# Kernel tuning notes

Hardware: AMD Instinct MI355X
Metric: run time of the kernel (lower is better)

## Reference

```python
import jax, jax.numpy as jnp
from jax import lax
import numpy as np

V, E, H, L, B, ML, T = 32000, 512, 512, 2, 64, 64, 32


def setup_inputs() -> dict:
    key = jax.random.key(0)
    ks = jax.random.split(key, 16)
    s = 0.05
    return {
        "current_input": jax.random.randint(ks[0], (B,), 0, V),
        "h0": jax.random.normal(ks[1], (L, B, H), jnp.float32),
        "c0": jax.random.normal(ks[2], (L, B, H), jnp.float32),
        "encoder_output": jax.random.normal(ks[3], (ML, B, H), jnp.float32),
        "gtruth": jax.random.randint(ks[4], (T, B), 0, V),
        "length": T,
        "emb": s * jax.random.normal(ks[5], (V, E), jnp.float32),
        "attn_W": s * jax.random.normal(ks[6], (ML, E + H), jnp.float32),
        "attn_out_W": s * jax.random.normal(ks[7], (E, E + H), jnp.float32),
        "lstm_Wi": s * jax.random.normal(ks[8], (L, 4 * H, E), jnp.float32),
        "lstm_Wh": s * jax.random.normal(ks[9], (L, 4 * H, H), jnp.float32),
        "lstm_bi": s * jax.random.normal(ks[10], (L, 4 * H), jnp.float32),
        "lstm_bh": s * jax.random.normal(ks[11], (L, 4 * H), jnp.float32),
        "gen_W": s * jax.random.normal(ks[12], (V, H), jnp.float32),
        "gen_b": s * jax.random.normal(ks[13], (V,), jnp.float32),
    }


def _lstm_cell(x, h, c, Wi, Wh, bi, bh):
    # PyTorch gate order: i, f, g, o
    g = x @ Wi.T + h @ Wh.T + bi + bh  # [B, 4H]
    i, f, gg, o = jnp.split(g, 4, axis=-1)
    c_new = jax.nn.sigmoid(f) * c + jax.nn.sigmoid(i) * jnp.tanh(gg)
    h_new = jax.nn.sigmoid(o) * jnp.tanh(c_new)
    return h_new, c_new


def reference(current_input, h0, c0, encoder_output, gtruth, length,
              emb, attn_W, attn_out_W, lstm_Wi, lstm_Wh, lstm_bi, lstm_bh,
              gen_W, gen_b):
    n_layers = h0.shape[0]

    def step_fn(carry, tok):
        h, c = carry  # each [L, B, H]
        emb_t = emb[tok]                                   # [B, E]
        attn_in = jnp.concatenate([emb_t, h[-1]], axis=1)  # [B, E+H]
        a = jax.nn.softmax(attn_in @ attn_W.T, axis=1)     # [B, ML]
        ctx = jnp.einsum('bl,lbh->bh', a, encoder_output)  # [B, H]
        rnn_in = jax.nn.relu(
            jnp.concatenate([emb_t, ctx], axis=1) @ attn_out_W.T)  # [B, E]
        x = rnn_in
        hs, cs = [], []
        for l in range(n_layers):
            hn, cn = _lstm_cell(x, h[l], c[l], lstm_Wi[l], lstm_Wh[l],
                                lstm_bi[l], lstm_bh[l])
            hs.append(hn)
            cs.append(cn)
            x = hn
        scores = x @ gen_W.T + gen_b  # [B, V]
        return (jnp.stack(hs), jnp.stack(cs)), scores

    # teacher forcing: step t consumes current_input at t=0, gtruth[t-1] after
    tokens = jnp.concatenate([current_input[None], gtruth[:-1]], axis=0)  # [T, B]
    (h_fin, c_fin), outputs = lax.scan(step_fn, (h0, c0), tokens)
    return outputs, h_fin, c_fin
```

## Files before the change

kernel.cpp:

```cpp
#include <hip/hip_runtime.h>
#include <hip/hip_bf16.h>

typedef __bf16 bf16_t;
typedef bf16_t bf16x8 __attribute__((ext_vector_type(8)));
typedef float f32x4 __attribute__((ext_vector_type(4)));

#define MFMA(a, b, c) __builtin_amdgcn_mfma_f32_16x16x32_bf16((a), (b), (c), 0, 0, 0)

__device__ __forceinline__ float sigm(float x) { return 1.f / (1.f + __expf(-x)); }
__device__ __forceinline__ float tanh_f(float x) { return 1.f - 2.f / (__expf(2.f * x) + 1.f); }

__device__ __forceinline__ bf16x8 cvt8(const float* p) {
    f32x4 a = *(const f32x4*)p, b = *(const f32x4*)(p + 4);
    bf16x8 v;
#pragma unroll
    for (int i = 0; i < 4; ++i) { v[i] = (bf16_t)a[i]; v[4 + i] = (bf16_t)b[i]; }
    return v;
}

__global__ void k_cvt(const float* __restrict__ src, bf16_t* __restrict__ dst, int n) {
    int i = (blockIdx.x * 256 + threadIdx.x) * 8;
    if (i < n) *(bf16x8*)(dst + i) = cvt8(src + i);
}

__global__ void k_init(const float* __restrict__ h0, const float* __restrict__ c0,
                       const float* __restrict__ bi, const float* __restrict__ bh,
                       float* __restrict__ c_f32, bf16_t* __restrict__ h_bf,
                       float* __restrict__ bsum) {
    int idx = blockIdx.x * 256 + threadIdx.x;
    if (idx < 65536) { c_f32[idx] = c0[idx]; h_bf[idx] = (bf16_t)h0[idx]; }
    if (idx < 4096) bsum[idx] = bi[idx] + bh[idx];
}

__global__ __launch_bounds__(256) void k_pre(const float* __restrict__ emb,
                                             const int* __restrict__ cur, const int* __restrict__ gt,
                                             const bf16_t* __restrict__ Bm, int ldb, int koff,
                                             float* __restrict__ out, int ldo) {
    int tid = threadIdx.x, lane = tid & 63, w = tid >> 6;
    int m = lane & 15, q = lane >> 4;
    int mrow = blockIdx.x * 64 + w * 16 + m;
    int tok = (mrow < 64) ? cur[mrow] : gt[mrow - 64];
    const float* arow = emb + (size_t)tok * 512;
    int n0 = blockIdx.y * 64;
    const bf16_t* brow0 = Bm + (size_t)(n0 + m) * ldb + koff;
    f32x4 acc[4] = {};
    for (int ks = 0; ks < 16; ++ks) {
        int kc = ks * 32 + q * 8;
        bf16x8 a = cvt8(arow + kc);
#pragma unroll
        for (int nt = 0; nt < 4; ++nt) {
            bf16x8 b = *(const bf16x8*)(brow0 + (size_t)nt * 16 * ldb + kc);
            acc[nt] = MFMA(a, b, acc[nt]);
        }
    }
    int rbase = blockIdx.x * 64 + w * 16 + q * 4;
#pragma unroll
    for (int nt = 0; nt < 4; ++nt)
#pragma unroll
        for (int i = 0; i < 4; ++i)
            out[(size_t)(rbase + i) * ldo + n0 + nt * 16 + m] = acc[nt][i];
}

__global__ __launch_bounds__(256) void k_attn_rnn(int t, const bf16_t* __restrict__ h2,
                                                  const bf16_t* __restrict__ attn_W,
                                                  const bf16_t* __restrict__ attn_out_W,
                                                  const float* __restrict__ enc,
                                                  const float* __restrict__ pre_s,
                                                  const float* __restrict__ pre_r,
                                                  bf16_t* __restrict__ rnn_bf) {
    __shared__ float s_p[8][64];
    __shared__ bf16_t s_ctx[16][520];
    int tid = threadIdx.x, lane = tid & 63, w = tid >> 6;
    int m = lane & 15, q = lane >> 4;
    int b0 = blockIdx.x * 8;
    for (int i = tid; i < 8 * 520; i += 256) s_ctx[8 + i / 520][i % 520] = (bf16_t)0.f;
    {
        const bf16_t* aptr = h2 + (size_t)(b0 + (m & 7)) * 512;
        const bf16_t* bptr = attn_W + (size_t)(w * 16 + m) * 1024 + 512;
        f32x4 acc = {};
        for (int ks = 0; ks < 16; ++ks) {
            int kc = ks * 32 + q * 8;
            acc = MFMA(*(const bf16x8*)(aptr + kc), *(const bf16x8*)(bptr + kc), acc);
        }
#pragma unroll
        for (int i = 0; i < 4; ++i) {
            int mr = q * 4 + i;
            if (mr < 8)
                s_p[mr][w * 16 + m] = acc[i] + pre_s[((size_t)t * 64 + b0 + mr) * 64 + w * 16 + m];
        }
    }
    __syncthreads();
    if (tid < 8) {
        float mx = -1e30f;
        for (int l = 0; l < 64; ++l) mx = fmaxf(mx, s_p[tid][l]);
        float sum = 0.f;
        for (int l = 0; l < 64; ++l) { float e = __expf(s_p[tid][l] - mx); s_p[tid][l] = e; sum += e; }
        float inv = 1.f / sum;
        for (int l = 0; l < 64; ++l) s_p[tid][l] *= inv;
    }
    __syncthreads();
    {
        int b = tid >> 5, g = tid & 31, h0 = g * 16;
        float acc[16];
#pragma unroll
        for (int i = 0; i < 16; ++i) acc[i] = 0.f;
        const float* ebase = enc + (size_t)(b0 + b) * 512 + h0;
        for (int l = 0; l < 64; ++l) {
            float a = s_p[b][l];
            const float* e = ebase + (size_t)l * 32768;
            f32x4 e0 = *(const f32x4*)(e), e1 = *(const f32x4*)(e + 4);
            f32x4 e2 = *(const f32x4*)(e + 8), e3 = *(const f32x4*)(e + 12);
#pragma unroll
            for (int i = 0; i < 4; ++i) {
                acc[i] += a * e0[i]; acc[4 + i] += a * e1[i];
                acc[8 + i] += a * e2[i]; acc[12 + i] += a * e3[i];
            }
        }
#pragma unroll
        for (int i = 0; i < 16; ++i) s_ctx[b][h0 + i] = (bf16_t)acc[i];
    }
    __syncthreads();
    {
        f32x4 acc[8] = {};
        const bf16_t* actx = &s_ctx[m][0];
        const bf16_t* bbase = attn_out_W + (size_t)(w * 128 + m) * 1024 + 512;
        for (int ks = 0; ks < 16; ++ks) {
            int kc = ks * 32 + q * 8;
            bf16x8 a = *(const bf16x8*)(actx + kc);
#pragma unroll
            for (int nt = 0; nt < 8; ++nt) {
                bf16x8 b = *(const bf16x8*)(bbase + (size_t)nt * 16 * 1024 + kc);
                acc[nt] = MFMA(a, b, acc[nt]);
            }
        }
#pragma unroll
        for (int nt = 0; nt < 8; ++nt)
#pragma unroll
            for (int i = 0; i < 4; ++i) {
                int mr = q * 4 + i;
                if (mr < 8) {
                    int b = b0 + mr, j = w * 128 + nt * 16 + m;
                    float v = acc[nt][i] + pre_r[((size_t)t * 64 + b) * 512 + j];
                    rnn_bf[(size_t)b * 512 + j] = (bf16_t)fmaxf(v, 0.f);
                }
            }
    }
}

__global__ __launch_bounds__(256) void k_lstm(const bf16_t* __restrict__ x,
                                              const bf16_t* __restrict__ hprev,
                                              const bf16_t* __restrict__ Wi,
                                              const bf16_t* __restrict__ Wh,
                                              const float* __restrict__ bsum,
                                              float* __restrict__ c,
                                              bf16_t* __restrict__ hout,
                                              bf16_t* __restrict__ xs_out) {
    int tid = threadIdx.x, lane = tid & 63, w = tid >> 6;
    int m = lane & 15, q = lane >> 4;
    int j0 = blockIdx.x * 16;
    const bf16_t* ax = x + (size_t)(w * 16 + m) * 512;
    const bf16_t* ah = hprev + (size_t)(w * 16 + m) * 512;
    f32x4 acc[4] = {};
    for (int ks = 0; ks < 16; ++ks) {
        int kc = ks * 32 + q * 8;
        bf16x8 a = *(const bf16x8*)(ax + kc);
#pragma unroll
        for (int g = 0; g < 4; ++g) {
            const bf16_t* bp = Wi + (size_t)(g * 512 + j0 + m) * 512 + kc;
            acc[g] = MFMA(a, *(const bf16x8*)bp, acc[g]);
        }
    }
    for (int ks = 0; ks < 16; ++ks) {
        int kc = ks * 32 + q * 8;
        bf16x8 a = *(const bf16x8*)(ah + kc);
#pragma unroll
        for (int g = 0; g < 4; ++g) {
            const bf16_t* bp = Wh + (size_t)(g * 512 + j0 + m) * 512 + kc;
            acc[g] = MFMA(a, *(const bf16x8*)bp, acc[g]);
        }
    }
    int j = j0 + m;
    float bs0 = bsum[j], bs1 = bsum[512 + j], bs2 = bsum[1024 + j], bs3 = bsum[1536 + j];
#pragma unroll
    for (int i = 0; i < 4; ++i) {
        int b = w * 16 + q * 4 + i;
        float ig = acc[0][i] + bs0;
        float fg = acc[1][i] + bs1;
        float gg = acc[2][i] + bs2;
        float og = acc[3][i] + bs3;
        size_t off = (size_t)b * 512 + j;
        float co = c[off];
        float cn = sigm(fg) * co + sigm(ig) * tanh_f(gg);
        float hn = sigm(og) * tanh_f(cn);
        c[off] = cn;
        hout[off] = (bf16_t)hn;
        if (xs_out) xs_out[off] = (bf16_t)hn;
    }
}

__global__ __launch_bounds__(256) void k_gen(const bf16_t* __restrict__ xs,
                                             const bf16_t* __restrict__ gen_W,
                                             const float* __restrict__ gen_b,
                                             float* __restrict__ out) {
    __shared__ bf16_t sA[64 * 256];
    int tid = threadIdx.x, lane = tid & 63, w = tid >> 6;
    int m = lane & 15, q4 = lane >> 4;
    int m0 = blockIdx.x * 64, n0 = blockIdx.y * 256;
    f32x4 acc[4][4] = {};
    for (int ko = 0; ko < 2; ++ko) {
        __syncthreads();
#pragma unroll
        for (int it = 0; it < 8; ++it) {
            int idx = it * 256 + tid;
            int mr = idx >> 5, qc = idx & 31;
            bf16x8 v = *(const bf16x8*)(xs + (size_t)(m0 + mr) * 512 + ko * 256 + qc * 8);
            *(bf16x8*)(&sA[(mr * 32 + (qc ^ (mr & 7))) * 8]) = v;
        }
        __syncthreads();
        const bf16_t* bbase = gen_W + (size_t)(n0 + w * 64 + m) * 512 + ko * 256;
        for (int ks = 0; ks < 8; ++ks) {
            bf16x8 af[4];
#pragma unroll
            for (int mt = 0; mt < 4; ++mt) {
                int r = mt * 16 + m, chunk = ks * 4 + q4;
                af[mt] = *(const bf16x8*)(&sA[(r * 32 + (chunk ^ (r & 7))) * 8]);
            }
            int kc = ks * 32 + q4 * 8;
#pragma unroll
            for (int nt = 0; nt < 4; ++nt) {
                bf16x8 bfrag = *(const bf16x8*)(bbase + (size_t)nt * 16 * 512 + kc);
#pragma unroll
                for (int mt = 0; mt < 4; ++mt) acc[mt][nt] = MFMA(af[mt], bfrag, acc[mt][nt]);
            }
        }
    }
#pragma unroll
    for (int nt = 0; nt < 4; ++nt) {
        int col = n0 + w * 64 + nt * 16 + m;
        float bias = gen_b[col];
#pragma unroll
        for (int mt = 0; mt < 4; ++mt)
#pragma unroll
            for (int i = 0; i < 4; ++i) {
                int r = m0 + mt * 16 + q4 * 4 + i;
                out[(size_t)r * 32000 + col] = acc[mt][nt][i] + bias;
            }
    }
}

__global__ void k_tail(const bf16_t* __restrict__ h_bf0, const float* __restrict__ c_f32,
                       float* __restrict__ out) {
    int idx = blockIdx.x * 256 + threadIdx.x;
    if (idx < 65536) {
        out[65536000 + idx] = (float)h_bf0[idx];
        out[65601536 + idx] = c_f32[idx];
    }
}

extern "C" void kernel_launch(void* const* d_in, const int* in_sizes, int n_in,
                              void* d_out, int out_size, void* d_ws, size_t ws_size,
                              hipStream_t stream) {
    const int* cur = (const int*)d_in[0];
    const float* h0 = (const float*)d_in[1];
    const float* c0 = (const float*)d_in[2];
    const float* enc = (const float*)d_in[3];
    const int* gt = (const int*)d_in[4];
    const float* emb = (const float*)d_in[6];
    const float* attn_W = (const float*)d_in[7];
    const float* attn_out_W = (const float*)d_in[8];
    const float* Wi = (const float*)d_in[9];
    const float* Wh = (const float*)d_in[10];
    const float* bi = (const float*)d_in[11];
    const float* bh = (const float*)d_in[12];
    const float* gen_W = (const float*)d_in[13];
    const float* gen_b = (const float*)d_in[14];
    float* out = (float*)d_out;

    char* ws = (char*)d_ws;
    float* c_f32 = (float*)(ws + 0);
    bf16_t* h_bf = (bf16_t*)(ws + 262144);
    float* bsum = (float*)(ws + 524288);
    float* pre_s = (float*)(ws + 540672);
    float* pre_r = (float*)(ws + 1064960);
    bf16_t* rnn_bf = (bf16_t*)(ws + 5259264);
    bf16_t* xs = (bf16_t*)(ws + 5324800);
    bf16_t* attn_W_bf = (bf16_t*)(ws + 7421952);
    bf16_t* attn_out_W_bf = (bf16_t*)(ws + 7553024);
    bf16_t* Wi_bf = (bf16_t*)(ws + 8601600);
    bf16_t* Wh_bf = (bf16_t*)(ws + 12795904);
    bf16_t* gen_W_bf = (bf16_t*)(ws + 16990208);

    k_cvt<<<32, 256, 0, stream>>>(attn_W, attn_W_bf, 65536);
    k_cvt<<<256, 256, 0, stream>>>(attn_out_W, attn_out_W_bf, 524288);
    k_cvt<<<1024, 256, 0, stream>>>(Wi, Wi_bf, 2097152);
    k_cvt<<<1024, 256, 0, stream>>>(Wh, Wh_bf, 2097152);
    k_cvt<<<8000, 256, 0, stream>>>(gen_W, gen_W_bf, 16384000);
    k_init<<<256, 256, 0, stream>>>(h0, c0, bi, bh, c_f32, h_bf, bsum);
    k_pre<<<dim3(32, 1), 256, 0, stream>>>(emb, cur, gt, attn_W_bf, 1024, 0, pre_s, 64);
    k_pre<<<dim3(32, 8), 256, 0, stream>>>(emb, cur, gt, attn_out_W_bf, 1024, 0, pre_r, 512);

    for (int t = 0; t < 32; ++t) {
        int p = t & 1;
        const bf16_t* hp = h_bf + (size_t)p * 65536;
        bf16_t* hn = h_bf + (size_t)(p ^ 1) * 65536;
        k_attn_rnn<<<8, 256, 0, stream>>>(t, hp + 32768, attn_W_bf, attn_out_W_bf, enc, pre_s, pre_r, rnn_bf);
        k_lstm<<<32, 256, 0, stream>>>(rnn_bf, hp, Wi_bf, Wh_bf, bsum, c_f32, hn, nullptr);
        k_lstm<<<32, 256, 0, stream>>>(hn, hp + 32768, Wi_bf + 1048576, Wh_bf + 1048576, bsum + 2048,
                                       c_f32 + 32768, hn + 32768, xs + (size_t)t * 32768);
    }
    k_gen<<<dim3(32, 125), 256, 0, stream>>>(xs, gen_W_bf, gen_b, out);
    k_tail<<<256, 256, 0, stream>>>(h_bf, c_f32, out);
}
```

Baseline: 3.295 ms.

## Fuse recurrent time loop into one persistent kernel with grid barriers

Replaces the 96 per-step kernel launches (attention, two LSTM layers) with a single persistent 32-block kernel. Blocks synchronize through an atomic-counter global barrier between phases. The attention work is repartitioned so each block handles 2 batch rows for softmax/context and a 16-column slice of the attn_out projection, with the context staged through a global buffer. It also uses wave shuffles for the softmax. This removes launch gaps and tail effects, at the cost of four grid-wide barriers per step and a reliance on all 32 blocks being co-resident.

```diff
diff --git a/kernel.cpp b/kernel.cpp
--- a/kernel.cpp
+++ b/kernel.cpp
@@ -3,6 +3,7 @@
 
 typedef __bf16 bf16_t;
 typedef bf16_t bf16x8 __attribute__((ext_vector_type(8)));
+typedef bf16_t bf16x4 __attribute__((ext_vector_type(4)));
 typedef float f32x4 __attribute__((ext_vector_type(4)));
 
 #define MFMA(a, b, c) __builtin_amdgcn_mfma_f32_16x16x32_bf16((a), (b), (c), 0, 0, 0)
@@ -18,6 +19,18 @@
     return v;
 }
 
+__device__ __forceinline__ void gbar(int* cnt, int target) {
+    __syncthreads();
+    if (threadIdx.x == 0) {
+        __threadfence();
+        __hip_atomic_fetch_add(cnt, 1, __ATOMIC_RELEASE, __HIP_MEMORY_SCOPE_AGENT);
+        while (__hip_atomic_load(cnt, __ATOMIC_ACQUIRE, __HIP_MEMORY_SCOPE_AGENT) < target)
+            __builtin_amdgcn_s_sleep(2);
+        __threadfence();
+    }
+    __syncthreads();
+}
+
 __global__ void k_cvt(const float* __restrict__ src, bf16_t* __restrict__ dst, int n) {
     int i = (blockIdx.x * 256 + threadIdx.x) * 8;
     if (i < n) *(bf16x8*)(dst + i) = cvt8(src + i);
@@ -26,10 +39,11 @@
 __global__ void k_init(const float* __restrict__ h0, const float* __restrict__ c0,
                        const float* __restrict__ bi, const float* __restrict__ bh,
                        float* __restrict__ c_f32, bf16_t* __restrict__ h_bf,
-                       float* __restrict__ bsum) {
+                       float* __restrict__ bsum, int* __restrict__ bar) {
     int idx = blockIdx.x * 256 + threadIdx.x;
     if (idx < 65536) { c_f32[idx] = c0[idx]; h_bf[idx] = (bf16_t)h0[idx]; }
     if (idx < 4096) bsum[idx] = bi[idx] + bh[idx];
+    if (idx == 0) *bar = 0;
 }
 
 __global__ __launch_bounds__(256) void k_pre(const float* __restrict__ emb,
@@ -61,103 +75,18 @@
             out[(size_t)(rbase + i) * ldo + n0 + nt * 16 + m] = acc[nt][i];
 }
 
-__global__ __launch_bounds__(256) void k_attn_rnn(int t, const bf16_t* __restrict__ h2,
-                                                  const bf16_t* __restrict__ attn_W,
-                                                  const bf16_t* __restrict__ attn_out_W,
-                                                  const float* __restrict__ enc,
-                                                  const float* __restrict__ pre_s,
-                                                  const float* __restrict__ pre_r,
-                                                  bf16_t* __restrict__ rnn_bf) {
-    __shared__ float s_p[8][64];
-    __shared__ bf16_t s_ctx[16][520];
-    int tid = threadIdx.x, lane = tid & 63, w = tid >> 6;
+__device__ __forceinline__ void lstm_phase(int wg, int tid,
+                                           const bf16_t* __restrict__ x,
+                                           const bf16_t* __restrict__ hprev,
+                                           const bf16_t* __restrict__ Wi,
+                                           const bf16_t* __restrict__ Wh,
+                                           const float* __restrict__ bsum,
+                                           float* __restrict__ c,
+                                           bf16_t* __restrict__ hout,
+                                           bf16_t* __restrict__ xs_out) {
+    int lane = tid & 63, w = tid >> 6;
     int m = lane & 15, q = lane >> 4;
-    int b0 = blockIdx.x * 8;
-    for (int i = tid; i < 8 * 520; i += 256) s_ctx[8 + i / 520][i % 520] = (bf16_t)0.f;
-    {
-        const bf16_t* aptr = h2 + (size_t)(b0 + (m & 7)) * 512;
-        const bf16_t* bptr = attn_W + (size_t)(w * 16 + m) * 1024 + 512;
-        f32x4 acc = {};
-        for (int ks = 0; ks < 16; ++ks) {
-            int kc = ks * 32 + q * 8;
-            acc = MFMA(*(const bf16x8*)(aptr + kc), *(const bf16x8*)(bptr + kc), acc);
-        }
-#pragma unroll
-        for (int i = 0; i < 4; ++i) {
-            int mr = q * 4 + i;
-            if (mr < 8)
-                s_p[mr][w * 16 + m] = acc[i] + pre_s[((size_t)t * 64 + b0 + mr) * 64 + w * 16 + m];
-        }
-    }
-    __syncthreads();
-    if (tid < 8) {
-        float mx = -1e30f;
-        for (int l = 0; l < 64; ++l) mx = fmaxf(mx, s_p[tid][l]);
-        float sum = 0.f;
-        for (int l = 0; l < 64; ++l) { float e = __expf(s_p[tid][l] - mx); s_p[tid][l] = e; sum += e; }
-        float inv = 1.f / sum;
-        for (int l = 0; l < 64; ++l) s_p[tid][l] *= inv;
-    }
-    __syncthreads();
-    {
-        int b = tid >> 5, g = tid & 31, h0 = g * 16;
-        float acc[16];
-#pragma unroll
-        for (int i = 0; i < 16; ++i) acc[i] = 0.f;
-        const float* ebase = enc + (size_t)(b0 + b) * 512 + h0;
-        for (int l = 0; l < 64; ++l) {
-            float a = s_p[b][l];
-            const float* e = ebase + (size_t)l * 32768;
-            f32x4 e0 = *(const f32x4*)(e), e1 = *(const f32x4*)(e + 4);
-            f32x4 e2 = *(const f32x4*)(e + 8), e3 = *(const f32x4*)(e + 12);
-#pragma unroll
-            for (int i = 0; i < 4; ++i) {
-                acc[i] += a * e0[i]; acc[4 + i] += a * e1[i];
-                acc[8 + i] += a * e2[i]; acc[12 + i] += a * e3[i];
-            }
-        }
-#pragma unroll
-        for (int i = 0; i < 16; ++i) s_ctx[b][h0 + i] = (bf16_t)acc[i];
-    }
-    __syncthreads();
-    {
-        f32x4 acc[8] = {};
-        const bf16_t* actx = &s_ctx[m][0];
-        const bf16_t* bbase = attn_out_W + (size_t)(w * 128 + m) * 1024 + 512;
-        for (int ks = 0; ks < 16; ++ks) {
-            int kc = ks * 32 + q * 8;
-            bf16x8 a = *(const bf16x8*)(actx + kc);
-#pragma unroll
-            for (int nt = 0; nt < 8; ++nt) {
-                bf16x8 b = *(const bf16x8*)(bbase + (size_t)nt * 16 * 1024 + kc);
-                acc[nt] = MFMA(a, b, acc[nt]);
-            }
-        }
-#pragma unroll
-        for (int nt = 0; nt < 8; ++nt)
-#pragma unroll
-            for (int i = 0; i < 4; ++i) {
-                int mr = q * 4 + i;
-                if (mr < 8) {
-                    int b = b0 + mr, j = w * 128 + nt * 16 + m;
-                    float v = acc[nt][i] + pre_r[((size_t)t * 64 + b) * 512 + j];
-                    rnn_bf[(size_t)b * 512 + j] = (bf16_t)fmaxf(v, 0.f);
-                }
-            }
-    }
-}
-
-__global__ __launch_bounds__(256) void k_lstm(const bf16_t* __restrict__ x,
-                                              const bf16_t* __restrict__ hprev,
-                                              const bf16_t* __restrict__ Wi,
-                                              const bf16_t* __restrict__ Wh,
-                                              const float* __restrict__ bsum,
-                                              float* __restrict__ c,
-                                              bf16_t* __restrict__ hout,
-                                              bf16_t* __restrict__ xs_out) {
-    int tid = threadIdx.x, lane = tid & 63, w = tid >> 6;
-    int m = lane & 15, q = lane >> 4;
-    int j0 = blockIdx.x * 16;
+    int j0 = wg * 16;
     const bf16_t* ax = x + (size_t)(w * 16 + m) * 512;
     const bf16_t* ah = hprev + (size_t)(w * 16 + m) * 512;
     f32x4 acc[4] = {};
@@ -195,6 +124,109 @@
         c[off] = cn;
         hout[off] = (bf16_t)hn;
         if (xs_out) xs_out[off] = (bf16_t)hn;
+    }
+}
+
+__global__ __launch_bounds__(256) void k_loop(const bf16_t* __restrict__ attn_W_bf,
+                                              const bf16_t* __restrict__ attn_out_W_bf,
+                                              const float* __restrict__ enc,
+                                              const float* __restrict__ pre_s,
+                                              const float* __restrict__ pre_r,
+                                              const bf16_t* __restrict__ Wi_bf,
+                                              const bf16_t* __restrict__ Wh_bf,
+                                              const float* __restrict__ bsum,
+                                              float* __restrict__ c_f32,
+                                              bf16_t* __restrict__ h_bf,
+                                              bf16_t* __restrict__ ctx_bf,
+                                              bf16_t* __restrict__ rnn_bf,
+                                              bf16_t* __restrict__ xs,
+                                              int* __restrict__ bar) {
+    __shared__ float s_p[2][64];
+    int tid = threadIdx.x, lane = tid & 63, w = tid >> 6;
+    int m = lane & 15, q = lane >> 4;
+    int wg = blockIdx.x;
+    int b0 = wg * 2;
+    int bt = 0;
+
+    for (int t = 0; t < 32; ++t) {
+        int p = t & 1;
+        const bf16_t* h1p = h_bf + (size_t)p * 65536;
+        const bf16_t* h2p = h1p + 32768;
+        bf16_t* h1n = h_bf + (size_t)(p ^ 1) * 65536;
+        bf16_t* h2n = h1n + 32768;
+
+        {
+            const bf16_t* aptr = h2p + (size_t)(b0 + (m & 1)) * 512;
+            const bf16_t* bptr = attn_W_bf + (size_t)(w * 16 + m) * 1024 + 512;
+            f32x4 acc = {};
+            for (int ks = 0; ks < 16; ++ks) {
+                int kc = ks * 32 + q * 8;
+                acc = MFMA(*(const bf16x8*)(aptr + kc), *(const bf16x8*)(bptr + kc), acc);
+            }
+            if (q == 0) {
+#pragma unroll
+                for (int i = 0; i < 2; ++i)
+                    s_p[i][w * 16 + m] =
+                        acc[i] + pre_s[((size_t)t * 64 + b0 + i) * 64 + w * 16 + m];
+            }
+        }
+        __syncthreads();
+        if (tid < 128) {
+            int r = tid >> 6, l = tid & 63;
+            float v = s_p[r][l];
+            float mx = v;
+#pragma unroll
+            for (int off = 32; off; off >>= 1) mx = fmaxf(mx, __shfl_xor(mx, off));
+            float e = __expf(v - mx);
+            float s = e;
+#pragma unroll
+            for (int off = 32; off; off >>= 1) s += __shfl_xor(s, off);
+            s_p[r][l] = e / s;
+        }
+        __syncthreads();
+        {
+            int r = tid >> 7, c0 = (tid & 127) * 4;
+            int b = b0 + r;
+            f32x4 acc = {};
+            const float* ebase = enc + (size_t)b * 512 + c0;
+            for (int l = 0; l < 64; ++l) {
+                float a = s_p[r][l];
+                f32x4 e = *(const f32x4*)(ebase + (size_t)l * 32768);
+#pragma unroll
+                for (int i = 0; i < 4; ++i) acc[i] += a * e[i];
+            }
+            bf16x4 cv;
+#pragma unroll
+            for (int i = 0; i < 4; ++i) cv[i] = (bf16_t)acc[i];
+            *(bf16x4*)(ctx_bf + (size_t)b * 512 + c0) = cv;
+        }
+        bt += 32; gbar(bar, bt);
+
+        {
+            int j0 = wg * 16;
+            const bf16_t* actx = ctx_bf + (size_t)(w * 16 + m) * 512;
+            const bf16_t* bptr = attn_out_W_bf + (size_t)(j0 + m) * 1024 + 512;
+            f32x4 acc = {};
+            for (int ks = 0; ks < 16; ++ks) {
+                int kc = ks * 32 + q * 8;
+                acc = MFMA(*(const bf16x8*)(actx + kc), *(const bf16x8*)(bptr + kc), acc);
+            }
+            int jj = j0 + m;
+#pragma unroll
+            for (int i = 0; i < 4; ++i) {
+                int b = w * 16 + q * 4 + i;
+                float v = acc[i] + pre_r[((size_t)t * 64 + b) * 512 + jj];
+                rnn_bf[(size_t)b * 512 + jj] = (bf16_t)fmaxf(v, 0.f);
+            }
+        }
+        bt += 32; gbar(bar, bt);
+
+        lstm_phase(wg, tid, rnn_bf, h1p, Wi_bf, Wh_bf, bsum, c_f32, h1n, nullptr);
+        bt += 32; gbar(bar, bt);
+
+        lstm_phase(wg, tid, h1n, h2p, Wi_bf + 1048576, Wh_bf + 1048576, bsum + 2048,
+                   c_f32 + 32768, h2n, xs + (size_t)t * 32768);
+        bt += 32; gbar(bar, bt);
     }
 }
 
@@ -289,25 +321,21 @@
     bf16_t* Wi_bf = (bf16_t*)(ws + 8601600);
     bf16_t* Wh_bf = (bf16_t*)(ws + 12795904);
     bf16_t* gen_W_bf = (bf16_t*)(ws + 16990208);
+    bf16_t* ctx_bf = (bf16_t*)(ws + 49758208);
+    int* bar = (int*)(ws + 49823744);
 
     k_cvt<<<32, 256, 0, stream>>>(attn_W, attn_W_bf, 65536);
     k_cvt<<<256, 256, 0, stream>>>(attn_out_W, attn_out_W_bf, 524288);
     k_cvt<<<1024, 256, 0, stream>>>(Wi, Wi_bf, 2097152);
     k_cvt<<<1024, 256, 0, stream>>>(Wh, Wh_bf, 2097152);
     k_cvt<<<8000, 256, 0, stream>>>(gen_W, gen_W_bf, 16384000);
-    k_init<<<256, 256, 0, stream>>>(h0, c0, bi, bh, c_f32, h_bf, bsum);
+    k_init<<<256, 256, 0, stream>>>(h0, c0, bi, bh, c_f32, h_bf, bsum, bar);
     k_pre<<<dim3(32, 1), 256, 0, stream>>>(emb, cur, gt, attn_W_bf, 1024, 0, pre_s, 64);
     k_pre<<<dim3(32, 8), 256, 0, stream>>>(emb, cur, gt, attn_out_W_bf, 1024, 0, pre_r, 512);
 
-    for (int t = 0; t < 32; ++t) {
-        int p = t & 1;
-        const bf16_t* hp = h_bf + (size_t)p * 65536;
-        bf16_t* hn = h_bf + (size_t)(p ^ 1) * 65536;
-        k_attn_rnn<<<8, 256, 0, stream>>>(t, hp + 32768, attn_W_bf, attn_out_W_bf, enc, pre_s, pre_r, rnn_bf);
-        k_lstm<<<32, 256, 0, stream>>>(rnn_bf, hp, Wi_bf, Wh_bf, bsum, c_f32, hn, nullptr);
-        k_lstm<<<32, 256, 0, stream>>>(hn, hp + 32768, Wi_bf + 1048576, Wh_bf + 1048576, bsum + 2048,
-                                       c_f32 + 32768, hn + 32768, xs + (size_t)t * 32768);
-    }
+    k_loop<<<32, 256, 0, stream>>>(attn_W_bf, attn_out_W_bf, enc, pre_s, pre_r,
+                                   Wi_bf, Wh_bf, bsum, c_f32, h_bf, ctx_bf, rnn_bf, xs, bar);
+
     k_gen<<<dim3(32, 125), 256, 0, stream>>>(xs, gen_W_bf, gen_b, out);
     k_tail<<<256, 256, 0, stream>>>(h_bf, c_f32, out);
 }
```

Measured after the change: 3.567 ms. 1.08x slower.
